# Kernel tuning notes

Measured on AMD Instinct MI355X. Metric: run time of the kernel, lower is better.

The kernel has to match this reference:

```python
import jax, jax.numpy as jnp
import numpy as np

N_NODES = 50000
N_FEATURES = 128
HIDDEN = 64
N_EDGES = 1600000


def gcn_conv(x, src, dst, edge_w, W, b, num_nodes):
    """torch_geometric GCNConv with edge weights: add self-loops (weight 1),
    symmetric deg^-1/2 normalization, aggregate into dst, then bias."""
    loop = jnp.arange(num_nodes)
    src_f = jnp.concatenate([src, loop])
    dst_f = jnp.concatenate([dst, loop])
    w_f = jnp.concatenate([edge_w, jnp.ones((num_nodes,), dtype=edge_w.dtype)])
    deg = jax.ops.segment_sum(w_f, dst_f, num_segments=num_nodes)
    dinv = jnp.where(deg > 0, jax.lax.rsqrt(deg), 0.0)
    norm = dinv[src_f] * w_f * dinv[dst_f]            # [E+N]
    h = x @ W                                          # [N, out]
    msg = h[src_f] * norm[:, None]                     # [E+N, out]
    out = jax.ops.segment_sum(msg, dst_f, num_segments=num_nodes)
    return out + b


def setup_inputs() -> dict:
    key = jax.random.key(0)
    ks = jax.random.split(key, 12)
    features = jax.random.normal(ks[0], (N_NODES, N_FEATURES), dtype=jnp.float32)
    edge_index = jax.random.randint(ks[1], (2, N_EDGES), 0, N_NODES, dtype=jnp.int64)
    edge_attr = jax.random.uniform(ks[2], (N_EDGES,), dtype=jnp.float32)
    s = 0.05
    W1 = jax.random.normal(ks[3], (N_FEATURES, HIDDEN), dtype=jnp.float32) * s
    b1 = jnp.zeros((HIDDEN,), dtype=jnp.float32)
    W2 = jax.random.normal(ks[4], (HIDDEN, HIDDEN // 2), dtype=jnp.float32) * s
    b2 = jnp.zeros((HIDDEN // 2,), dtype=jnp.float32)
    Wd = jax.random.normal(ks[5], (N_FEATURES, 2), dtype=jnp.float32) * s
    bd = jnp.zeros((2,), dtype=jnp.float32)
    w_fc = jax.random.normal(ks[6], (N_NODES * 2,), dtype=jnp.float32) * s
    b_fc = jnp.zeros((), dtype=jnp.float32)
    return {"features": features, "edge_index": edge_index, "edge_attr": edge_attr,
            "W1": W1, "b1": b1, "W2": W2, "b2": b2, "Wd": Wd, "bd": bd,
            "w_fc": w_fc, "b_fc": b_fc}


def reference(features, edge_index, edge_attr, W1, b1, W2, b2, Wd, bd, w_fc, b_fc):
    N = features.shape[0]
    src, dst = edge_index[0], edge_index[1]
    # --- generator encoder (GAE.encode): GCN -> relu -> GCN -> tanh ---
    h = gcn_conv(features, src, dst, edge_attr, W1, b1, N)
    h = jax.nn.relu(h)                                  # dropout inactive (eval)
    z = jnp.tanh(gcn_conv(h, src, dst, edge_attr, W2, b2, N))  # [N, HIDDEN//2]
    # --- residual path: tile z to n_features width and add input features ---
    rep = features.shape[1] // z.shape[1]
    x = jnp.tile(z, (1, rep)) + features                # [N, n_features]
    # (edge_probabilities = z@z.T + rebuilt adjacency is computed by the
    #  generator but discarded by GraphCounteRGAN.forward -> dead code)
    # --- discriminator: GCN -> relu -> flatten -> fc -> sigmoid ---
    d = jax.nn.relu(gcn_conv(x, src, dst, edge_attr, Wd, bd, N))  # [N, 2]
    logit = jnp.dot(d.reshape(-1), w_fc) + b_fc
    return jax.nn.sigmoid(logit)
```

## Files before the change

kernel.cpp:

```cpp
#include <hip/hip_runtime.h>
#include <math.h>

#define BLK 256
#define CHUNK 4096
#define BSH 8
#define BNODES 256
#define MAXNB 256

__device__ __forceinline__ unsigned short f2bf(float f) {
    unsigned u = __float_as_uint(f);
    u += 0x7FFFu + ((u >> 16) & 1u);
    return (unsigned short)(u >> 16);
}
__device__ __forceinline__ float bf2f(unsigned short b) {
    return __uint_as_float(((unsigned)b) << 16);
}

__global__ void detect_kernel(const int* __restrict__ idx, int E,
                              int* __restrict__ flag, float* __restrict__ acc,
                              int* __restrict__ done) {
    int t = threadIdx.x;
    long long j = (long long)t * (E / 64);
    int hi = idx[2 * j + 1];
    unsigned long long b = __ballot(hi != 0);
    if (t == 0) { *flag = (b == 0ULL) ? 1 : 0; *acc = 0.f; *done = 0; }
}

__global__ __launch_bounds__(256) void bucket_hist_kernel(const int* __restrict__ idx,
                                                          int* __restrict__ blockCnt,
                                                          int E, int NB) {
    __shared__ int hist[MAXNB];
    __shared__ int i64s;
    int t = threadIdx.x;
    for (int i = t; i < NB; i += 256) hist[i] = 0;
    if (t < 64) {
        long long j = (long long)t * (E / 64);
        int hi = idx[2 * j + 1];
        unsigned long long b = __ballot(hi != 0);
        if (t == 0) i64s = (b == 0ULL) ? 1 : 0;
    }
    __syncthreads();
    bool i64 = i64s != 0;
    int e0 = blockIdx.x * CHUNK;
    int e1 = min(e0 + CHUNK, E);
    for (int e = e0 + t; e < e1; e += 256) {
        int d = i64 ? idx[2 * (E + e)] : idx[E + e];
        atomicAdd(&hist[d >> BSH], 1);
    }
    __syncthreads();
    for (int i = t; i < NB; i += 256) blockCnt[blockIdx.x * NB + i] = hist[i];
}

__global__ __launch_bounds__(256) void col_scan_kernel(const int* __restrict__ blockCnt,
                                                       int* __restrict__ blockBase,
                                                       int* __restrict__ bucketTotal,
                                                       int NBLK, int NB) {
    __shared__ int s[256];
    __shared__ int carry;
    int bkt = blockIdx.x;
    int t = threadIdx.x;
    if (t == 0) carry = 0;
    __syncthreads();
    for (int base = 0; base < NBLK; base += 256) {
        int i = base + t;
        int v = (i < NBLK) ? blockCnt[i * NB + bkt] : 0;
        s[t] = v;
        __syncthreads();
        for (int off = 1; off < 256; off <<= 1) {
            int x = (t >= off) ? s[t - off] : 0;
            __syncthreads();
            s[t] += x;
            __syncthreads();
        }
        if (i < NBLK) blockBase[i * NB + bkt] = carry + s[t] - v;
        __syncthreads();
        if (t == 0) carry += s[255];
        __syncthreads();
    }
    if (t == 0) bucketTotal[bkt] = carry;
}

__global__ __launch_bounds__(256) void bucket_scan_kernel(const int* __restrict__ bucketTotal,
                                                          int* __restrict__ bucketBase, int NB,
                                                          float* __restrict__ acc,
                                                          int* __restrict__ done) {
    __shared__ int s[256];
    int t = threadIdx.x;
    if (t == 0) { *acc = 0.f; *done = 0; }
    int v = (t < NB) ? bucketTotal[t] : 0;
    s[t] = v;
    __syncthreads();
    for (int off = 1; off < 256; off <<= 1) {
        int x = (t >= off) ? s[t - off] : 0;
        __syncthreads();
        s[t] += x;
        __syncthreads();
    }
    if (t < NB) bucketBase[t] = s[t] - v;
}

__global__ __launch_bounds__(256) void bucket_scatter_kernel(const int* __restrict__ idx,
                                                             const float* __restrict__ ew,
                                                             const int* __restrict__ bucketBase,
                                                             const int* __restrict__ blockBase,
                                                             int2* __restrict__ temp,
                                                             int E, int NB) {
    __shared__ int base[MAXNB];
    __shared__ int fill[MAXNB];
    __shared__ int i64s;
    int t = threadIdx.x;
    for (int i = t; i < NB; i += 256) {
        base[i] = bucketBase[i] + blockBase[blockIdx.x * NB + i];
        fill[i] = 0;
    }
    if (t < 64) {
        long long j = (long long)t * (E / 64);
        int hi = idx[2 * j + 1];
        unsigned long long b = __ballot(hi != 0);
        if (t == 0) i64s = (b == 0ULL) ? 1 : 0;
    }
    __syncthreads();
    bool i64 = i64s != 0;
    int e0 = blockIdx.x * CHUNK;
    int e1 = min(e0 + CHUNK, E);
    for (int e = e0 + t; e < e1; e += 256) {
        int s_, d;
        if (i64) { s_ = idx[2 * e]; d = idx[2 * (E + e)]; }
        else     { s_ = idx[e];     d = idx[E + e]; }
        float w = ew[e];
        int b = d >> BSH;
        int pos = base[b] + atomicAdd(&fill[b], 1);
        temp[pos] = make_int2(s_ | ((d & (BNODES - 1)) << 16), __float_as_int(w));
    }
}

__global__ __launch_bounds__(512) void csr_build_kernel(const int2* __restrict__ temp,
                                                        const int* __restrict__ bucketBase,
                                                        unsigned* __restrict__ csrw,
                                                        int* __restrict__ row,
                                                        float* __restrict__ dinv,
                                                        int N, int NB, int E) {
    __shared__ int cnt[BNODES];
    __shared__ float dw[BNODES];
    __shared__ int offs[BNODES];
    int bkt = blockIdx.x;
    int t = threadIdx.x;
    int node0 = bkt << BSH;
    int nn = min(BNODES, N - node0);
    if (t < BNODES) { cnt[t] = 0; dw[t] = 0.f; }
    __syncthreads();
    int p0 = bucketBase[bkt];
    int p1 = (bkt + 1 < NB) ? bucketBase[bkt + 1] : E;
    for (int p = p0 + t; p < p1; p += 512) {
        int2 v = temp[p];
        int dl = (v.x >> 16) & (BNODES - 1);
        atomicAdd(&cnt[dl], 1);
        atomicAdd(&dw[dl], __int_as_float(v.y));
    }
    __syncthreads();
    int v = 0;
    if (t < BNODES) { v = cnt[t]; offs[t] = v; }
    __syncthreads();
    for (int off = 1; off < BNODES; off <<= 1) {
        int x = 0;
        if (t < BNODES && t >= off) x = offs[t - off];
        __syncthreads();
        if (t < BNODES) offs[t] += x;
        __syncthreads();
    }
    if (t < BNODES) {
        int excl = offs[t] - v;
        if (t < nn) {
            row[node0 + t] = p0 + excl;
            dinv[node0 + t] = rsqrtf(1.f + dw[t]);
        }
        offs[t] = excl;
    }
    if (bkt == NB - 1 && t == 0) row[N] = E;
    __syncthreads();
    if (t < BNODES) cnt[t] = 0;
    __syncthreads();
    for (int p = p0 + t; p < p1; p += 512) {
        int2 v2 = temp[p];
        int dl = (v2.x >> 16) & (BNODES - 1);
        int pos = p0 + offs[dl] + atomicAdd(&cnt[dl], 1);
        unsigned wb = (unsigned)v2.y;
        wb += 0x7FFFu + ((wb >> 16) & 1u);
        csrw[pos] = ((unsigned)v2.x & 0xFFFFu) | (wb & 0xFFFF0000u);
    }
}

__global__ void norm_kernel(unsigned* __restrict__ csrw, const float* __restrict__ dinv, int E) {
    int e = blockIdx.x * BLK + threadIdx.x;
    if (e >= E) return;
    unsigned pe = csrw[e];
    float w = __uint_as_float(pe & 0xFFFF0000u) * dinv[pe & 0xFFFFu];
    unsigned wb = __float_as_uint(w);
    wb += 0x7FFFu + ((wb >> 16) & 1u);
    csrw[e] = (pe & 0xFFFFu) | (wb & 0xFFFF0000u);
}

__global__ __launch_bounds__(256) void gather64_kernel(const int* __restrict__ row,
                                                       const unsigned* __restrict__ csrw,
                                                       const unsigned short* __restrict__ h,
                                                       const float* __restrict__ dinv,
                                                       const float* __restrict__ bias,
                                                       float* __restrict__ out, int N) {
    int wid = (blockIdx.x * 256 + threadIdx.x) >> 6;
    int o = threadIdx.x & 63;
    if (wid >= N) return;
    float di = dinv[wid];
    int p0 = row[wid], p1 = row[wid + 1];
    const unsigned short* hb = h + o;
    float es[4] = {0.f, 0.f, 0.f, 0.f};
    for (int p = p0; p < p1; p += 64) {
        int q = p + o;
        unsigned pe = (q < p1) ? csrw[q] : 0u;
        int m = min(64, p1 - p);
        int mp = (m + 15) & ~15;
        for (int j = 0; j < mp; j += 16) {
            unsigned ee[16];
            float hh[16];
#pragma unroll
            for (int u = 0; u < 16; ++u) ee[u] = (unsigned)__shfl((int)pe, j + u, 64);
#pragma unroll
            for (int u = 0; u < 16; ++u) hh[u] = bf2f(hb[(ee[u] & 0xFFFFu) * 64]);
#pragma unroll
            for (int u = 0; u < 16; ++u)
                es[u & 3] = fmaf(__uint_as_float(ee[u] & 0xFFFF0000u), hh[u], es[u & 3]);
        }
    }
    float e01 = es[0] + es[1], e23 = es[2] + es[3];
    out[wid * 64 + o] = bias[o] + di * (di * bf2f(h[(size_t)wid * 64 + o]) + e01 + e23);
}

__global__ __launch_bounds__(256) void gather32_kernel(const int* __restrict__ row,
                                                       const unsigned* __restrict__ csrw,
                                                       const unsigned short* __restrict__ h,
                                                       const float* __restrict__ dinv,
                                                       const float* __restrict__ bias,
                                                       float* __restrict__ out, int N) {
    int wid = (blockIdx.x * 256 + threadIdx.x) >> 6;
    int lane = threadIdx.x & 63;
    int o = lane & 31;
    int g = lane >> 5;
    if (wid >= N) return;
    float di = dinv[wid];
    int p0 = row[wid], p1 = row[wid + 1];
    const unsigned short* hb = h + o;
    float es[4] = {0.f, 0.f, 0.f, 0.f};
    for (int p = p0; p < p1; p += 64) {
        int q = p + lane;
        unsigned pe = (q < p1) ? csrw[q] : 0u;
        int m = min(64, p1 - p);
        int mp = (m + 15) & ~15;
        for (int j = g; j < mp; j += 16) {
            unsigned ee[8];
            float hh[8];
#pragma unroll
            for (int u = 0; u < 8; ++u) ee[u] = (unsigned)__shfl((int)pe, j + 2 * u, 64);
#pragma unroll
            for (int u = 0; u < 8; ++u) hh[u] = bf2f(hb[(ee[u] & 0xFFFFu) * 32]);
#pragma unroll
            for (int u = 0; u < 8; ++u)
                es[u & 3] = fmaf(__uint_as_float(ee[u] & 0xFFFF0000u), hh[u], es[u & 3]);
        }
    }
    float es_t = (es[0] + es[1]) + (es[2] + es[3]);
    es_t += __shfl_down(es_t, 32, 64);
    if (g == 0) out[wid * 32 + o] = bias[o] + di * (di * bf2f(h[wid * 32 + o]) + es_t);
}

__global__ __launch_bounds__(256) void gather2_kernel(const int* __restrict__ row,
                                                      const unsigned* __restrict__ csrw,
                                                      const unsigned short* __restrict__ h,
                                                      const float* __restrict__ dinv,
                                                      const float* __restrict__ bias,
                                                      float* __restrict__ out, int N) {
    const unsigned* hp = (const unsigned*)h;
    int wid = (blockIdx.x * 256 + threadIdx.x) >> 6;
    int lane = threadIdx.x & 63;
    if (wid >= N) return;
    float di = dinv[wid];
    int p0 = row[wid], p1 = row[wid + 1];
    float a0 = 0.f, a1 = 0.f, b0 = 0.f, b1 = 0.f;
    int p = p0 + lane;
    for (; p + 64 < p1; p += 128) {
        unsigned pe0 = csrw[p];
        unsigned pe1 = csrw[p + 64];
        unsigned hw0 = hp[pe0 & 0xFFFFu];
        unsigned hw1 = hp[pe1 & 0xFFFFu];
        float w0 = __uint_as_float(pe0 & 0xFFFF0000u);
        float w1 = __uint_as_float(pe1 & 0xFFFF0000u);
        a0 = fmaf(w0, __uint_as_float(hw0 << 16), a0);
        a1 = fmaf(w0, __uint_as_float(hw0 & 0xFFFF0000u), a1);
        b0 = fmaf(w1, __uint_as_float(hw1 << 16), b0);
        b1 = fmaf(w1, __uint_as_float(hw1 & 0xFFFF0000u), b1);
    }
    if (p < p1) {
        unsigned pe0 = csrw[p];
        unsigned hw0 = hp[pe0 & 0xFFFFu];
        float w0 = __uint_as_float(pe0 & 0xFFFF0000u);
        a0 = fmaf(w0, __uint_as_float(hw0 << 16), a0);
        a1 = fmaf(w0, __uint_as_float(hw0 & 0xFFFF0000u), a1);
    }
    a0 += b0; a1 += b1;
#pragma unroll
    for (int off = 32; off > 0; off >>= 1) {
        a0 += __shfl_down(a0, off, 64);
        a1 += __shfl_down(a1, off, 64);
    }
    if (lane == 0) {
        unsigned hw = hp[wid];
        out[wid * 2 + 0] = bias[0] + di * (di * __uint_as_float(hw << 16) + a0);
        out[wid * 2 + 1] = bias[1] + di * (di * __uint_as_float(hw & 0xFFFF0000u) + a1);
    }
}

__global__ __launch_bounds__(256) void mm1_kernel(const float* __restrict__ X,
                                                  const float* __restrict__ W,
                                                  unsigned short* __restrict__ Y, int N) {
    __shared__ float Xs[32 * 132];
    __shared__ uint2 Wsb[128 * 16];
    const float4* Wg = (const float4*)W;
    for (int i = threadIdx.x; i < 128 * 16; i += 256) {
        float4 wv = Wg[i];
        unsigned lo = ((unsigned)f2bf(wv.x)) | (((unsigned)f2bf(wv.y)) << 16);
        unsigned hi = ((unsigned)f2bf(wv.z)) | (((unsigned)f2bf(wv.w)) << 16);
        Wsb[i] = make_uint2(lo, hi);
    }
    int row0 = blockIdx.x * 32;
    for (int i = threadIdx.x; i < 32 * 128; i += 256) {
        int r = i >> 7, k = i & 127;
        int rr = row0 + r;
        Xs[r * 132 + k] = (rr < N) ? X[(size_t)rr * 128 + k] : 0.f;
    }
    __syncthreads();
    int r0 = (threadIdx.x >> 4) * 2;
    int c4 = threadIdx.x & 15;
    float4 a0 = {0.f, 0.f, 0.f, 0.f};
    float4 a1 = {0.f, 0.f, 0.f, 0.f};
#pragma unroll 4
    for (int k = 0; k < 128; ++k) {
        float x0 = Xs[r0 * 132 + k];
        float x1 = Xs[(r0 + 1) * 132 + k];
        uint2 wp = Wsb[k * 16 + c4];
        float w0 = __uint_as_float(wp.x << 16);
        float w1 = __uint_as_float(wp.x & 0xFFFF0000u);
        float w2 = __uint_as_float(wp.y << 16);
        float w3 = __uint_as_float(wp.y & 0xFFFF0000u);
        a0.x = fmaf(x0, w0, a0.x); a0.y = fmaf(x0, w1, a0.y);
        a0.z = fmaf(x0, w2, a0.z); a0.w = fmaf(x0, w3, a0.w);
        a1.x = fmaf(x1, w0, a1.x); a1.y = fmaf(x1, w1, a1.y);
        a1.z = fmaf(x1, w2, a1.z); a1.w = fmaf(x1, w3, a1.w);
    }
    int row = row0 + r0;
    if (row < N) {
        ushort4 o;
        o.x = f2bf(a0.x); o.y = f2bf(a0.y); o.z = f2bf(a0.z); o.w = f2bf(a0.w);
        ((ushort4*)Y)[(size_t)row * 16 + c4] = o;
    }
    if (row + 1 < N) {
        ushort4 o;
        o.x = f2bf(a1.x); o.y = f2bf(a1.y); o.z = f2bf(a1.z); o.w = f2bf(a1.w);
        ((ushort4*)Y)[(size_t)(row + 1) * 16 + c4] = o;
    }
}

__global__ __launch_bounds__(256) void mm2_kernel(const float* __restrict__ H,
                                                  const float* __restrict__ W,
                                                  unsigned short* __restrict__ Y, int N) {
    __shared__ float Xs[32 * 68];
    __shared__ float4 Ws[64 * 8];
    const float4* Wg = (const float4*)W;
    for (int i = threadIdx.x; i < 64 * 8; i += 256) Ws[i] = Wg[i];
    int row0 = blockIdx.x * 32;
    for (int i = threadIdx.x; i < 32 * 64; i += 256) {
        int r = i >> 6, k = i & 63;
        int row = row0 + r;
        Xs[r * 68 + k] = (row < N) ? fmaxf(H[row * 64 + k], 0.f) : 0.f;
    }
    __syncthreads();
    int r = threadIdx.x >> 3;
    int c4 = threadIdx.x & 7;
    int row = row0 + r;
    float4 acc = {0.f, 0.f, 0.f, 0.f};
#pragma unroll 4
    for (int k = 0; k < 64; ++k) {
        float xv = Xs[r * 68 + k];
        float4 wv = Ws[k * 8 + c4];
        acc.x = fmaf(xv, wv.x, acc.x);
        acc.y = fmaf(xv, wv.y, acc.y);
        acc.z = fmaf(xv, wv.z, acc.z);
        acc.w = fmaf(xv, wv.w, acc.w);
    }
    if (row < N) {
        ushort4 o;
        o.x = f2bf(acc.x); o.y = f2bf(acc.y); o.z = f2bf(acc.z); o.w = f2bf(acc.w);
        ((ushort4*)Y)[row * 8 + c4] = o;
    }
}

__global__ __launch_bounds__(256) void disc_mm_kernel(const float* __restrict__ Z,
                                                      const float* __restrict__ F,
                                                      const float* __restrict__ Wd,
                                                      unsigned short* __restrict__ Y, int N) {
    __shared__ float Ws[256];
    if (threadIdx.x < 256) Ws[threadIdx.x] = Wd[threadIdx.x];
    __syncthreads();
    int n = blockIdx.x * 256 + threadIdx.x;
    if (n >= N) return;
    float zt[32];
#pragma unroll
    for (int j = 0; j < 32; ++j) zt[j] = tanhf(Z[n * 32 + j]);
    float a0 = 0.f, a1 = 0.f;
    const float* fr = F + (size_t)n * 128;
#pragma unroll 4
    for (int c = 0; c < 128; ++c) {
        float xv = zt[c & 31] + fr[c];
        a0 = fmaf(xv, Ws[c * 2 + 0], a0);
        a1 = fmaf(xv, Ws[c * 2 + 1], a1);
    }
    ushort2 o;
    o.x = f2bf(a0); o.y = f2bf(a1);
    ((ushort2*)Y)[n] = o;
}

__global__ void init_deg_kernel(float* __restrict__ deg, int N) {
    int n = blockIdx.x * BLK + threadIdx.x;
    if (n < N) deg[n] = 1.0f;
}

__global__ void edge_deg_kernel(const int* __restrict__ idx, const float* __restrict__ ew,
                                const int* __restrict__ flag, float* __restrict__ deg, int E) {
    int e = blockIdx.x * BLK + threadIdx.x;
    if (e >= E) return;
    int d = (*flag) ? idx[2 * (E + e)] : idx[E + e];
    atomicAdd(&deg[d], ew[e]);
}

__global__ void dinv_kernel(float* __restrict__ deg, int N) {
    int n = blockIdx.x * BLK + threadIdx.x;
    if (n < N) deg[n] = rsqrtf(deg[n]);
}

template <int WD>
__global__ void init_agg_kernel(const unsigned short* __restrict__ h, const float* __restrict__ dinv,
                                const float* __restrict__ bias, float* __restrict__ agg, int N) {
    int i = blockIdx.x * BLK + threadIdx.x;
    if (i >= N * WD) return;
    int n = i / WD, o = i % WD;
    float di = dinv[n];
    agg[i] = bias[o] + di * di * bf2f(h[i]);
}

template <int WD>
__global__ void edge_agg_kernel(const int* __restrict__ idx, const float* __restrict__ ew,
                                const int* __restrict__ flag, const float* __restrict__ dinv,
                                const unsigned short* __restrict__ h, float* __restrict__ agg, int E) {
    int gid = blockIdx.x * BLK + threadIdx.x;
    if (gid >= E * WD) return;
    int e = gid / WD;
    int o = gid % WD;
    int s, d;
    if (*flag) { s = idx[2 * e]; d = idx[2 * (E + e)]; }
    else       { s = idx[e];     d = idx[E + e]; }
    float nrm = dinv[s] * ew[e] * dinv[d];
    atomicAdd(&agg[d * WD + o], nrm * bf2f(h[s * WD + o]));
}

__global__ void reduce_final_kernel(const float* __restrict__ dmat, const float* __restrict__ wfc,
                                    float* __restrict__ acc, int* __restrict__ done,
                                    const float* __restrict__ bfc, float* __restrict__ out,
                                    int M, int nblk) {
    int i = blockIdx.x * BLK + threadIdx.x;
    float v = 0.f;
    if (i < M) v = fmaxf(dmat[i], 0.f) * wfc[i];
#pragma unroll
    for (int off = 32; off > 0; off >>= 1) v += __shfl_down(v, off, 64);
    if ((threadIdx.x & 63) == 0) atomicAdd(acc, v);
    __syncthreads();
    if (threadIdx.x == 0) {
        __threadfence();
        int old = atomicAdd(done, 1);
        if (old == nblk - 1) {
            float x = atomicAdd(acc, 0.f) + *bfc;
            out[0] = 1.f / (1.f + expf(-x));
        }
    }
}

extern "C" void kernel_launch(void* const* d_in, const int* in_sizes, int n_in,
                              void* d_out, int out_size, void* d_ws, size_t ws_size,
                              hipStream_t stream) {
    const float* feat = (const float*)d_in[0];
    const int*   eidx = (const int*)d_in[1];
    const float* ew   = (const float*)d_in[2];
    const float* W1   = (const float*)d_in[3];
    const float* b1   = (const float*)d_in[4];
    const float* W2   = (const float*)d_in[5];
    const float* b2   = (const float*)d_in[6];
    const float* Wd   = (const float*)d_in[7];
    const float* bd   = (const float*)d_in[8];
    const float* wfc  = (const float*)d_in[9];
    const float* bfc  = (const float*)d_in[10];

    const int N = in_sizes[0] / 128;
    const int E = in_sizes[2];

    const int NB   = (N + BNODES - 1) >> BSH;
    const int NBLK = (E + CHUNK - 1) / CHUNK;

    float* ws = (float*)d_ws;
    size_t u = 0;
    float* dinv = ws + u; u += N;
    if (u & 1) u++;
    size_t M1 = ((size_t)N * 32 > (size_t)E * 2) ? (size_t)N * 32 : (size_t)E * 2;
    unsigned short* h = (unsigned short*)(ws + u); int2* temp = (int2*)h; u += M1;
    if (u & 1) u++;
    float* agg = ws + u; u += (size_t)N * 64;
    float* acc = ws + u; u += 1;
    int* flag = (int*)(ws + u); u += 1;
    int* done = (int*)(ws + u); u += 1;
    int* row  = (int*)(ws + u); u += (size_t)N + 1;
    int* bucketTotal = (int*)(ws + u); u += NB;
    int* bucketBase  = (int*)(ws + u); u += NB + 1;
    int* blockCnt    = (int*)(ws + u); u += (size_t)NBLK * NB;
    int* blockBase   = (int*)(ws + u); u += (size_t)NBLK * NB;
    unsigned* csrw   = (unsigned*)(ws + u); u += (size_t)E;
    size_t need = u * 4;

    float* out = (float*)d_out;

    const int gN = (N + BLK - 1) / BLK;
    const int gE = (E + BLK - 1) / BLK;
    const int gW = (N + 3) / 4;
    const int gR = (N * 2 + BLK - 1) / BLK;

    if (ws_size >= need && N <= 65536 && NB <= MAXNB) {
        hipLaunchKernelGGL(bucket_hist_kernel, dim3(NBLK), dim3(256), 0, stream,
                           eidx, blockCnt, E, NB);
        hipLaunchKernelGGL(col_scan_kernel, dim3(NB), dim3(256), 0, stream,
                           blockCnt, blockBase, bucketTotal, NBLK, NB);
        hipLaunchKernelGGL(bucket_scan_kernel, dim3(1), dim3(256), 0, stream,
                           bucketTotal, bucketBase, NB, acc, done);
        hipLaunchKernelGGL(bucket_scatter_kernel, dim3(NBLK), dim3(256), 0, stream,
                           eidx, ew, bucketBase, blockBase, temp, E, NB);
        hipLaunchKernelGGL(csr_build_kernel, dim3(NB), dim3(512), 0, stream,
                           temp, bucketBase, csrw, row, dinv, N, NB, E);
        hipLaunchKernelGGL(norm_kernel, dim3(gE), dim3(BLK), 0, stream, csrw, dinv, E);

        hipLaunchKernelGGL(mm1_kernel, dim3((N + 31) / 32), dim3(256), 0, stream, feat, W1, h, N);
        hipLaunchKernelGGL(gather64_kernel, dim3(gW), dim3(256), 0, stream,
                           row, csrw, h, dinv, b1, agg, N);
        hipLaunchKernelGGL(mm2_kernel, dim3((N + 31) / 32), dim3(256), 0, stream, agg, W2, h, N);
        hipLaunchKernelGGL(gather32_kernel, dim3(gW), dim3(256), 0, stream,
                           row, csrw, h, dinv, b2, agg, N);
        hipLaunchKernelGGL(disc_mm_kernel, dim3((N + 255) / 256), dim3(256), 0, stream,
                           agg, feat, Wd, h, N);
        hipLaunchKernelGGL(gather2_kernel, dim3(gW), dim3(256), 0, stream,
                           row, csrw, h, dinv, bd, agg, N);
    } else {
        hipLaunchKernelGGL(detect_kernel, dim3(1), dim3(64), 0, stream, eidx, E, flag, acc, done);
        hipLaunchKernelGGL(init_deg_kernel, dim3(gN), dim3(BLK), 0, stream, dinv, N);
        hipLaunchKernelGGL(edge_deg_kernel, dim3(gE), dim3(BLK), 0, stream, eidx, ew, flag, dinv, E);
        hipLaunchKernelGGL(dinv_kernel, dim3(gN), dim3(BLK), 0, stream, dinv, N);

        hipLaunchKernelGGL(mm1_kernel, dim3((N + 31) / 32), dim3(256), 0, stream, feat, W1, h, N);
        hipLaunchKernelGGL((init_agg_kernel<64>), dim3((N * 64 + BLK - 1) / BLK), dim3(BLK), 0, stream,
                           h, dinv, b1, agg, N);
        hipLaunchKernelGGL((edge_agg_kernel<64>), dim3((E / BLK) * 64 + 64), dim3(BLK), 0, stream,
                           eidx, ew, flag, dinv, h, agg, E);
        hipLaunchKernelGGL(mm2_kernel, dim3((N + 31) / 32), dim3(256), 0, stream, agg, W2, h, N);
        hipLaunchKernelGGL((init_agg_kernel<32>), dim3((N * 32 + BLK - 1) / BLK), dim3(BLK), 0, stream,
                           h, dinv, b2, agg, N);
        hipLaunchKernelGGL((edge_agg_kernel<32>), dim3((E / BLK) * 32 + 32), dim3(BLK), 0, stream,
                           eidx, ew, flag, dinv, h, agg, E);
        hipLaunchKernelGGL(disc_mm_kernel, dim3((N + 255) / 256), dim3(256), 0, stream,
                           agg, feat, Wd, h, N);
        hipLaunchKernelGGL((init_agg_kernel<2>), dim3((N * 2 + BLK - 1) / BLK), dim3(BLK), 0, stream,
                           h, dinv, bd, agg, N);
        hipLaunchKernelGGL((edge_agg_kernel<2>), dim3((E * 2 + BLK - 1) / BLK), dim3(BLK), 0, stream,
                           eidx, ew, flag, dinv, h, agg, E);
    }

    hipLaunchKernelGGL(reduce_final_kernel, dim3(gR), dim3(BLK), 0, stream,
                       agg, wfc, acc, done, bfc, out, N * 2, gR);
}
```

Before: 298.5 us.

## Fold source-side normalization into matmuls, use MFMA, drop norm and scan kernels

Each matmul output row is now pre-scaled by dinv of its source node, so the separate pass that multiplied CSR edge weights by dinv[src] is removed and the gather kernels skip the extra di factor on the self-loop term. The two small dense matmuls are rewritten with bf16 MFMA 16x16x32 instructions instead of scalar FMAs. The single-block bucket scan kernel is removed: each scatter and CSR-build block recomputes the prefix over bucket totals itself, and the acc/done reset moves into col_scan. This trades two launches and one full pass over the edge array for redundant small scans per block and bf16 rounding of the matmul inputs.

```diff
diff --git a/kernel.cpp b/kernel.cpp
--- a/kernel.cpp
+++ b/kernel.cpp
@@ -6,6 +6,9 @@
 #define BSH 8
 #define BNODES 256
 #define MAXNB 256
+
+typedef __attribute__((ext_vector_type(8))) short bf8_t;
+typedef __attribute__((ext_vector_type(4))) float f4_t;
 
 __device__ __forceinline__ unsigned short f2bf(float f) {
     unsigned u = __float_as_uint(f);
@@ -54,11 +57,14 @@
 __global__ __launch_bounds__(256) void col_scan_kernel(const int* __restrict__ blockCnt,
                                                        int* __restrict__ blockBase,
                                                        int* __restrict__ bucketTotal,
-                                                       int NBLK, int NB) {
+                                                       int NBLK, int NB,
+                                                       float* __restrict__ acc,
+                                                       int* __restrict__ done) {
     __shared__ int s[256];
     __shared__ int carry;
     int bkt = blockIdx.x;
     int t = threadIdx.x;
+    if (bkt == 0 && t == 0) { *acc = 0.f; *done = 0; }
     if (t == 0) carry = 0;
     __syncthreads();
     for (int base = 0; base < NBLK; base += 256) {
@@ -80,44 +86,35 @@
     if (t == 0) bucketTotal[bkt] = carry;
 }
 
-__global__ __launch_bounds__(256) void bucket_scan_kernel(const int* __restrict__ bucketTotal,
-                                                          int* __restrict__ bucketBase, int NB,
-                                                          float* __restrict__ acc,
-                                                          int* __restrict__ done) {
-    __shared__ int s[256];
-    int t = threadIdx.x;
-    if (t == 0) { *acc = 0.f; *done = 0; }
-    int v = (t < NB) ? bucketTotal[t] : 0;
-    s[t] = v;
-    __syncthreads();
-    for (int off = 1; off < 256; off <<= 1) {
-        int x = (t >= off) ? s[t - off] : 0;
-        __syncthreads();
-        s[t] += x;
-        __syncthreads();
-    }
-    if (t < NB) bucketBase[t] = s[t] - v;
-}
-
 __global__ __launch_bounds__(256) void bucket_scatter_kernel(const int* __restrict__ idx,
                                                              const float* __restrict__ ew,
-                                                             const int* __restrict__ bucketBase,
+                                                             const int* __restrict__ bucketTotal,
                                                              const int* __restrict__ blockBase,
                                                              int2* __restrict__ temp,
                                                              int E, int NB) {
     __shared__ int base[MAXNB];
     __shared__ int fill[MAXNB];
+    __shared__ int s[256];
     __shared__ int i64s;
     int t = threadIdx.x;
-    for (int i = t; i < NB; i += 256) {
-        base[i] = bucketBase[i] + blockBase[blockIdx.x * NB + i];
-        fill[i] = 0;
-    }
+    int v = (t < NB) ? bucketTotal[t] : 0;
+    s[t] = v;
     if (t < 64) {
         long long j = (long long)t * (E / 64);
         int hi = idx[2 * j + 1];
         unsigned long long b = __ballot(hi != 0);
         if (t == 0) i64s = (b == 0ULL) ? 1 : 0;
+    }
+    __syncthreads();
+    for (int off = 1; off < 256; off <<= 1) {
+        int x = (t >= off) ? s[t - off] : 0;
+        __syncthreads();
+        s[t] += x;
+        __syncthreads();
+    }
+    if (t < NB) {
+        base[t] = (s[t] - v) + blockBase[blockIdx.x * NB + t];
+        fill[t] = 0;
     }
     __syncthreads();
     bool i64 = i64s != 0;
@@ -135,7 +132,7 @@
 }
 
 __global__ __launch_bounds__(512) void csr_build_kernel(const int2* __restrict__ temp,
-                                                        const int* __restrict__ bucketBase,
+                                                        const int* __restrict__ bucketTotal,
                                                         unsigned* __restrict__ csrw,
                                                         int* __restrict__ row,
                                                         float* __restrict__ dinv,
@@ -143,14 +140,23 @@
     __shared__ int cnt[BNODES];
     __shared__ float dw[BNODES];
     __shared__ int offs[BNODES];
+    __shared__ int sb[256];
     int bkt = blockIdx.x;
     int t = threadIdx.x;
     int node0 = bkt << BSH;
     int nn = min(BNODES, N - node0);
     if (t < BNODES) { cnt[t] = 0; dw[t] = 0.f; }
-    __syncthreads();
-    int p0 = bucketBase[bkt];
-    int p1 = (bkt + 1 < NB) ? bucketBase[bkt + 1] : E;
+    if (t < 256) sb[t] = (t < NB) ? bucketTotal[t] : 0;
+    __syncthreads();
+    for (int off = 1; off < 256; off <<= 1) {
+        int x = 0;
+        if (t < 256 && t >= off) x = sb[t - off];
+        __syncthreads();
+        if (t < 256) sb[t] += x;
+        __syncthreads();
+    }
+    int p0 = (bkt > 0) ? sb[bkt - 1] : 0;
+    int p1 = sb[bkt];
     for (int p = p0 + t; p < p1; p += 512) {
         int2 v = temp[p];
         int dl = (v.x >> 16) & (BNODES - 1);
@@ -188,16 +194,6 @@
         wb += 0x7FFFu + ((wb >> 16) & 1u);
         csrw[pos] = ((unsigned)v2.x & 0xFFFFu) | (wb & 0xFFFF0000u);
     }
-}
-
-__global__ void norm_kernel(unsigned* __restrict__ csrw, const float* __restrict__ dinv, int E) {
-    int e = blockIdx.x * BLK + threadIdx.x;
-    if (e >= E) return;
-    unsigned pe = csrw[e];
-    float w = __uint_as_float(pe & 0xFFFF0000u) * dinv[pe & 0xFFFFu];
-    unsigned wb = __float_as_uint(w);
-    wb += 0x7FFFu + ((wb >> 16) & 1u);
-    csrw[e] = (pe & 0xFFFFu) | (wb & 0xFFFF0000u);
 }
 
 __global__ __launch_bounds__(256) void gather64_kernel(const int* __restrict__ row,
@@ -231,7 +227,7 @@
         }
     }
     float e01 = es[0] + es[1], e23 = es[2] + es[3];
-    out[wid * 64 + o] = bias[o] + di * (di * bf2f(h[(size_t)wid * 64 + o]) + e01 + e23);
+    out[wid * 64 + o] = bias[o] + di * (bf2f(h[(size_t)wid * 64 + o]) + e01 + e23);
 }
 
 __global__ __launch_bounds__(256) void gather32_kernel(const int* __restrict__ row,
@@ -268,7 +264,7 @@
     }
     float es_t = (es[0] + es[1]) + (es[2] + es[3]);
     es_t += __shfl_down(es_t, 32, 64);
-    if (g == 0) out[wid * 32 + o] = bias[o] + di * (di * bf2f(h[wid * 32 + o]) + es_t);
+    if (g == 0) out[wid * 32 + o] = bias[o] + di * (bf2f(h[wid * 32 + o]) + es_t);
 }
 
 __global__ __launch_bounds__(256) void gather2_kernel(const int* __restrict__ row,
@@ -312,98 +308,127 @@
     }
     if (lane == 0) {
         unsigned hw = hp[wid];
-        out[wid * 2 + 0] = bias[0] + di * (di * __uint_as_float(hw << 16) + a0);
-        out[wid * 2 + 1] = bias[1] + di * (di * __uint_as_float(hw & 0xFFFF0000u) + a1);
-    }
-}
-
-__global__ __launch_bounds__(256) void mm1_kernel(const float* __restrict__ X,
-                                                  const float* __restrict__ W,
-                                                  unsigned short* __restrict__ Y, int N) {
-    __shared__ float Xs[32 * 132];
-    __shared__ uint2 Wsb[128 * 16];
-    const float4* Wg = (const float4*)W;
-    for (int i = threadIdx.x; i < 128 * 16; i += 256) {
-        float4 wv = Wg[i];
-        unsigned lo = ((unsigned)f2bf(wv.x)) | (((unsigned)f2bf(wv.y)) << 16);
-        unsigned hi = ((unsigned)f2bf(wv.z)) | (((unsigned)f2bf(wv.w)) << 16);
-        Wsb[i] = make_uint2(lo, hi);
-    }
-    int row0 = blockIdx.x * 32;
-    for (int i = threadIdx.x; i < 32 * 128; i += 256) {
-        int r = i >> 7, k = i & 127;
-        int rr = row0 + r;
-        Xs[r * 132 + k] = (rr < N) ? X[(size_t)rr * 128 + k] : 0.f;
-    }
-    __syncthreads();
-    int r0 = (threadIdx.x >> 4) * 2;
-    int c4 = threadIdx.x & 15;
-    float4 a0 = {0.f, 0.f, 0.f, 0.f};
-    float4 a1 = {0.f, 0.f, 0.f, 0.f};
-#pragma unroll 4
-    for (int k = 0; k < 128; ++k) {
-        float x0 = Xs[r0 * 132 + k];
-        float x1 = Xs[(r0 + 1) * 132 + k];
-        uint2 wp = Wsb[k * 16 + c4];
-        float w0 = __uint_as_float(wp.x << 16);
-        float w1 = __uint_as_float(wp.x & 0xFFFF0000u);
-        float w2 = __uint_as_float(wp.y << 16);
-        float w3 = __uint_as_float(wp.y & 0xFFFF0000u);
-        a0.x = fmaf(x0, w0, a0.x); a0.y = fmaf(x0, w1, a0.y);
-        a0.z = fmaf(x0, w2, a0.z); a0.w = fmaf(x0, w3, a0.w);
-        a1.x = fmaf(x1, w0, a1.x); a1.y = fmaf(x1, w1, a1.y);
-        a1.z = fmaf(x1, w2, a1.z); a1.w = fmaf(x1, w3, a1.w);
-    }
-    int row = row0 + r0;
-    if (row < N) {
-        ushort4 o;
-        o.x = f2bf(a0.x); o.y = f2bf(a0.y); o.z = f2bf(a0.z); o.w = f2bf(a0.w);
-        ((ushort4*)Y)[(size_t)row * 16 + c4] = o;
-    }
-    if (row + 1 < N) {
-        ushort4 o;
-        o.x = f2bf(a1.x); o.y = f2bf(a1.y); o.z = f2bf(a1.z); o.w = f2bf(a1.w);
-        ((ushort4*)Y)[(size_t)(row + 1) * 16 + c4] = o;
-    }
-}
-
-__global__ __launch_bounds__(256) void mm2_kernel(const float* __restrict__ H,
-                                                  const float* __restrict__ W,
-                                                  unsigned short* __restrict__ Y, int N) {
-    __shared__ float Xs[32 * 68];
-    __shared__ float4 Ws[64 * 8];
-    const float4* Wg = (const float4*)W;
-    for (int i = threadIdx.x; i < 64 * 8; i += 256) Ws[i] = Wg[i];
-    int row0 = blockIdx.x * 32;
-    for (int i = threadIdx.x; i < 32 * 64; i += 256) {
-        int r = i >> 6, k = i & 63;
-        int row = row0 + r;
-        Xs[r * 68 + k] = (row < N) ? fmaxf(H[row * 64 + k], 0.f) : 0.f;
-    }
-    __syncthreads();
-    int r = threadIdx.x >> 3;
-    int c4 = threadIdx.x & 7;
-    int row = row0 + r;
-    float4 acc = {0.f, 0.f, 0.f, 0.f};
-#pragma unroll 4
-    for (int k = 0; k < 64; ++k) {
-        float xv = Xs[r * 68 + k];
-        float4 wv = Ws[k * 8 + c4];
-        acc.x = fmaf(xv, wv.x, acc.x);
-        acc.y = fmaf(xv, wv.y, acc.y);
-        acc.z = fmaf(xv, wv.z, acc.z);
-        acc.w = fmaf(xv, wv.w, acc.w);
-    }
-    if (row < N) {
-        ushort4 o;
-        o.x = f2bf(acc.x); o.y = f2bf(acc.y); o.z = f2bf(acc.z); o.w = f2bf(acc.w);
-        ((ushort4*)Y)[row * 8 + c4] = o;
+        out[wid * 2 + 0] = bias[0] + di * (__uint_as_float(hw << 16) + a0);
+        out[wid * 2 + 1] = bias[1] + di * (__uint_as_float(hw & 0xFFFF0000u) + a1);
+    }
+}
+
+__global__ __launch_bounds__(256) void mm1_mfma_kernel(const float* __restrict__ X,
+                                                       const float* __restrict__ W,
+                                                       const float* __restrict__ dinv,
+                                                       unsigned short* __restrict__ Y, int N) {
+    __shared__ unsigned short Wf[4 * 4 * 64 * 8];
+    int t = threadIdx.x;
+    for (int i = t; i < 8192; i += 256) {
+        int j = i & 7;
+        int lane = (i >> 3) & 63;
+        int ct = (i >> 9) & 3;
+        int kt = i >> 11;
+        int k = kt * 32 + (lane >> 4) * 8 + j;
+        int c = ct * 16 + (lane & 15);
+        Wf[i] = f2bf(W[k * 64 + c]);
+    }
+    __syncthreads();
+    int wave = t >> 6, lane = t & 63;
+    int row0 = blockIdx.x * 64 + wave * 16;
+    if (row0 >= N) return;
+    int r = row0 + (lane & 15);
+    int kq = (lane >> 4) * 8;
+    bool rv = r < N;
+    f4_t acc0 = {0.f, 0.f, 0.f, 0.f}, acc1 = acc0, acc2 = acc0, acc3 = acc0;
+    const bf8_t* wf = (const bf8_t*)Wf;
+#pragma unroll
+    for (int kt = 0; kt < 4; ++kt) {
+        bf8_t a = {0, 0, 0, 0, 0, 0, 0, 0};
+        if (rv) {
+            const float4* ap = (const float4*)(X + (size_t)r * 128 + kt * 32 + kq);
+            float4 lo = ap[0], hi = ap[1];
+            a[0] = (short)f2bf(lo.x); a[1] = (short)f2bf(lo.y);
+            a[2] = (short)f2bf(lo.z); a[3] = (short)f2bf(lo.w);
+            a[4] = (short)f2bf(hi.x); a[5] = (short)f2bf(hi.y);
+            a[6] = (short)f2bf(hi.z); a[7] = (short)f2bf(hi.w);
+        }
+        bf8_t b0 = wf[(kt * 4 + 0) * 64 + lane];
+        bf8_t b1 = wf[(kt * 4 + 1) * 64 + lane];
+        bf8_t b2 = wf[(kt * 4 + 2) * 64 + lane];
+        bf8_t b3 = wf[(kt * 4 + 3) * 64 + lane];
+        acc0 = __builtin_amdgcn_mfma_f32_16x16x32_bf16(a, b0, acc0, 0, 0, 0);
+        acc1 = __builtin_amdgcn_mfma_f32_16x16x32_bf16(a, b1, acc1, 0, 0, 0);
+        acc2 = __builtin_amdgcn_mfma_f32_16x16x32_bf16(a, b2, acc2, 0, 0, 0);
+        acc3 = __builtin_amdgcn_mfma_f32_16x16x32_bf16(a, b3, acc3, 0, 0, 0);
+    }
+    int colb = lane & 15;
+    int rbase = row0 + (lane >> 4) * 4;
+#pragma unroll
+    for (int reg = 0; reg < 4; ++reg) {
+        int rr = rbase + reg;
+        if (rr < N) {
+            float dv = dinv[rr];
+            Y[(size_t)rr * 64 + colb]      = f2bf(dv * acc0[reg]);
+            Y[(size_t)rr * 64 + 16 + colb] = f2bf(dv * acc1[reg]);
+            Y[(size_t)rr * 64 + 32 + colb] = f2bf(dv * acc2[reg]);
+            Y[(size_t)rr * 64 + 48 + colb] = f2bf(dv * acc3[reg]);
+        }
+    }
+}
+
+__global__ __launch_bounds__(256) void mm2_mfma_kernel(const float* __restrict__ A,
+                                                       const float* __restrict__ W,
+                                                       const float* __restrict__ dinv,
+                                                       unsigned short* __restrict__ Y, int N) {
+    __shared__ unsigned short Wf[2 * 2 * 64 * 8];
+    int t = threadIdx.x;
+    for (int i = t; i < 2048; i += 256) {
+        int j = i & 7;
+        int lane = (i >> 3) & 63;
+        int ct = (i >> 9) & 1;
+        int kt = i >> 10;
+        int k = kt * 32 + (lane >> 4) * 8 + j;
+        int c = ct * 16 + (lane & 15);
+        Wf[i] = f2bf(W[k * 32 + c]);
+    }
+    __syncthreads();
+    int wave = t >> 6, lane = t & 63;
+    int row0 = blockIdx.x * 64 + wave * 16;
+    if (row0 >= N) return;
+    int r = row0 + (lane & 15);
+    int kq = (lane >> 4) * 8;
+    bool rv = r < N;
+    f4_t acc0 = {0.f, 0.f, 0.f, 0.f}, acc1 = acc0;
+    const bf8_t* wf = (const bf8_t*)Wf;
+#pragma unroll
+    for (int kt = 0; kt < 2; ++kt) {
+        bf8_t a = {0, 0, 0, 0, 0, 0, 0, 0};
+        if (rv) {
+            const float4* ap = (const float4*)(A + (size_t)r * 64 + kt * 32 + kq);
+            float4 lo = ap[0], hi = ap[1];
+            a[0] = (short)f2bf(fmaxf(lo.x, 0.f)); a[1] = (short)f2bf(fmaxf(lo.y, 0.f));
+            a[2] = (short)f2bf(fmaxf(lo.z, 0.f)); a[3] = (short)f2bf(fmaxf(lo.w, 0.f));
+            a[4] = (short)f2bf(fmaxf(hi.x, 0.f)); a[5] = (short)f2bf(fmaxf(hi.y, 0.f));
+            a[6] = (short)f2bf(fmaxf(hi.z, 0.f)); a[7] = (short)f2bf(fmaxf(hi.w, 0.f));
+        }
+        bf8_t b0 = wf[(kt * 2 + 0) * 64 + lane];
+        bf8_t b1 = wf[(kt * 2 + 1) * 64 + lane];
+        acc0 = __builtin_amdgcn_mfma_f32_16x16x32_bf16(a, b0, acc0, 0, 0, 0);
+        acc1 = __builtin_amdgcn_mfma_f32_16x16x32_bf16(a, b1, acc1, 0, 0, 0);
+    }
+    int colb = lane & 15;
+    int rbase = row0 + (lane >> 4) * 4;
+#pragma unroll
+    for (int reg = 0; reg < 4; ++reg) {
+        int rr = rbase + reg;
+        if (rr < N) {
+            float dv = dinv[rr];
+            Y[(size_t)rr * 32 + colb]      = f2bf(dv * acc0[reg]);
+            Y[(size_t)rr * 32 + 16 + colb] = f2bf(dv * acc1[reg]);
+        }
     }
 }
 
 __global__ __launch_bounds__(256) void disc_mm_kernel(const float* __restrict__ Z,
                                                       const float* __restrict__ F,
                                                       const float* __restrict__ Wd,
+                                                      const float* __restrict__ dinv,
                                                       unsigned short* __restrict__ Y, int N) {
     __shared__ float Ws[256];
     if (threadIdx.x < 256) Ws[threadIdx.x] = Wd[threadIdx.x];
@@ -421,8 +446,9 @@
         a0 = fmaf(xv, Ws[c * 2 + 0], a0);
         a1 = fmaf(xv, Ws[c * 2 + 1], a1);
     }
+    float dv = dinv[n];
     ushort2 o;
-    o.x = f2bf(a0); o.y = f2bf(a1);
+    o.x = f2bf(dv * a0); o.y = f2bf(dv * a1);
     ((ushort2*)Y)[n] = o;
 }
 
@@ -451,7 +477,7 @@
     if (i >= N * WD) return;
     int n = i / WD, o = i % WD;
     float di = dinv[n];
-    agg[i] = bias[o] + di * di * bf2f(h[i]);
+    agg[i] = bias[o] + di * bf2f(h[i]);
 }
 
 template <int WD>
@@ -465,7 +491,7 @@
     int s, d;
     if (*flag) { s = idx[2 * e]; d = idx[2 * (E + e)]; }
     else       { s = idx[e];     d = idx[E + e]; }
-    float nrm = dinv[s] * ew[e] * dinv[d];
+    float nrm = ew[e] * dinv[d];
     atomicAdd(&agg[d * WD + o], nrm * bf2f(h[s * WD + o]));
 }
 
@@ -524,7 +550,6 @@
     int* done = (int*)(ws + u); u += 1;
     int* row  = (int*)(ws + u); u += (size_t)N + 1;
     int* bucketTotal = (int*)(ws + u); u += NB;
-    int* bucketBase  = (int*)(ws + u); u += NB + 1;
     int* blockCnt    = (int*)(ws + u); u += (size_t)NBLK * NB;
     int* blockBase   = (int*)(ws + u); u += (size_t)NBLK * NB;
     unsigned* csrw   = (unsigned*)(ws + u); u += (size_t)E;
@@ -535,29 +560,29 @@
     const int gN = (N + BLK - 1) / BLK;
     const int gE = (E + BLK - 1) / BLK;
     const int gW = (N + 3) / 4;
+    const int gM = (N + 63) / 64;
     const int gR = (N * 2 + BLK - 1) / BLK;
 
     if (ws_size >= need && N <= 65536 && NB <= MAXNB) {
         hipLaunchKernelGGL(bucket_hist_kernel, dim3(NBLK), dim3(256), 0, stream,
                            eidx, blockCnt, E, NB);
         hipLaunchKernelGGL(col_scan_kernel, dim3(NB), dim3(256), 0, stream,
-                           blockCnt, blockBase, bucketTotal, NBLK, NB);
-        hipLaunchKernelGGL(bucket_scan_kernel, dim3(1), dim3(256), 0, stream,
-                           bucketTotal, bucketBase, NB, acc, done);
+                           blockCnt, blockBase, bucketTotal, NBLK, NB, acc, done);
         hipLaunchKernelGGL(bucket_scatter_kernel, dim3(NBLK), dim3(256), 0, stream,
-                           eidx, ew, bucketBase, blockBase, temp, E, NB);
+                           eidx, ew, bucketTotal, blockBase, temp, E, NB);
         hipLaunchKernelGGL(csr_build_kernel, dim3(NB), dim3(512), 0, stream,
-                           temp, bucketBase, csrw, row, dinv, N, NB, E);
-        hipLaunchKernelGGL(norm_kernel, dim3(gE), dim3(BLK), 0, stream, csrw, dinv, E);
-
-        hipLaunchKernelGGL(mm1_kernel, dim3((N + 31) / 32), dim3(256), 0, stream, feat, W1, h, N);
+                           temp, bucketTotal, csrw, row, dinv, N, NB, E);
+
+        hipLaunchKernelGGL(mm1_mfma_kernel, dim3(gM), dim3(256), 0, stream,
+                           feat, W1, dinv, h, N);
         hipLaunchKernelGGL(gather64_kernel, dim3(gW), dim3(256), 0, stream,
                            row, csrw, h, dinv, b1, agg, N);
-        hipLaunchKernelGGL(mm2_kernel, dim3((N + 31) / 32), dim3(256), 0, stream, agg, W2, h, N);
+        hipLaunchKernelGGL(mm2_mfma_kernel, dim3(gM), dim3(256), 0, stream,
+                           agg, W2, dinv, h, N);
         hipLaunchKernelGGL(gather32_kernel, dim3(gW), dim3(256), 0, stream,
                            row, csrw, h, dinv, b2, agg, N);
         hipLaunchKernelGGL(disc_mm_kernel, dim3((N + 255) / 256), dim3(256), 0, stream,
-                           agg, feat, Wd, h, N);
+                           agg, feat, Wd, dinv, h, N);
         hipLaunchKernelGGL(gather2_kernel, dim3(gW), dim3(256), 0, stream,
                            row, csrw, h, dinv, bd, agg, N);
     } else {
@@ -566,18 +591,18 @@
         hipLaunchKernelGGL(edge_deg_kernel, dim3(gE), dim3(BLK), 0, stream, eidx, ew, flag, dinv, E);
         hipLaunchKernelGGL(dinv_kernel, dim3(gN), dim3(BLK), 0, stream, dinv, N);
 
-        hipLaunchKernelGGL(mm1_kernel, dim3((N + 31) / 32), dim3(256), 0, stream, feat, W1, h, N);
+        hipLaunchKernelGGL(mm1_mfma_kernel, dim3(gM), dim3(256), 0, stream, feat, W1, dinv, h, N);
         hipLaunchKernelGGL((init_agg_kernel<64>), dim3((N * 64 + BLK - 1) / BLK), dim3(BLK), 0, stream,
                            h, dinv, b1, agg, N);
         hipLaunchKernelGGL((edge_agg_kernel<64>), dim3((E / BLK) * 64 + 64), dim3(BLK), 0, stream,
                            eidx, ew, flag, dinv, h, agg, E);
-        hipLaunchKernelGGL(mm2_kernel, dim3((N + 31) / 32), dim3(256), 0, stream, agg, W2, h, N);
+        hipLaunchKernelGGL(mm2_mfma_kernel, dim3(gM), dim3(256), 0, stream, agg, W2, dinv, h, N);
         hipLaunchKernelGGL((init_agg_kernel<32>), dim3((N * 32 + BLK - 1) / BLK), dim3(BLK), 0, stream,
                            h, dinv, b2, agg, N);
         hipLaunchKernelGGL((edge_agg_kernel<32>), dim3((E / BLK) * 32 + 32), dim3(BLK), 0, stream,
                            eidx, ew, flag, dinv, h, agg, E);
         hipLaunchKernelGGL(disc_mm_kernel, dim3((N + 255) / 256), dim3(256), 0, stream,
-                           agg, feat, Wd, h, N);
+                           agg, feat, Wd, dinv, h, N);
         hipLaunchKernelGGL((init_agg_kernel<2>), dim3((N * 2 + BLK - 1) / BLK), dim3(BLK), 0, stream,
                            h, dinv, bd, agg, N);
         hipLaunchKernelGGL((edge_agg_kernel<2>), dim3((E * 2 + BLK - 1) / BLK), dim3(BLK), 0, stream,
```

After: 272.1 us. 1.1x faster.
